# Kernel tuning notes

Hardware: AMD Instinct MI355X
Metric: run time of the kernel (lower is better)

Reference implementation:

```python
import jax, jax.numpy as jnp
import numpy as np

B, CI, HW, K, C, NH, L = 512, 3, 28, 28 // 28 and 0 or 7, 1024, 16, 12
K = 7


def setup_inputs() -> dict:
    key = jax.random.key(0)
    ks = jax.random.split(key, 8)
    s = 0.02
    return {
        "x": jax.random.normal(ks[0], (B, CI, HW, HW), jnp.float32),
        "conv_w": jax.random.normal(ks[1], (C, CI, K, K), jnp.float32) * s,  # Conv2d weight [Co,Ci,k,k], shared with deconv
        "ln1_w": jnp.ones((L, C), jnp.float32),
        "ln1_b": jnp.zeros((L, C), jnp.float32),
        "wq": jax.random.normal(ks[2], (L, C, C), jnp.float32) * s,
        "wk": jax.random.normal(ks[3], (L, C, C), jnp.float32) * s,
        "wv": jax.random.normal(ks[4], (L, C, C), jnp.float32) * s,
        "ln2_w": jnp.ones((L, C), jnp.float32),
        "ln2_b": jnp.zeros((L, C), jnp.float32),
        "mlp_w": jax.random.normal(ks[5], (L, C, C), jnp.float32) * s,
        "mlp_b": jnp.zeros((L, C), jnp.float32),
        "out_w": jax.random.normal(ks[6], (C, C), jnp.float32) * s,
        "out_b": jnp.zeros((C,), jnp.float32),
        "head_num": NH,
    }


def _layernorm(x, w, b, eps=1e-5):
    m = jnp.mean(x, axis=-1, keepdims=True)
    v = jnp.var(x, axis=-1, keepdims=True)  # biased var, matches torch LayerNorm
    return (x - m) * jax.lax.rsqrt(v + eps) * w + b


def _attn(h, wq, wk, wv, nh):
    b, t, c = h.shape
    hd = c // nh
    q = (h @ wq.T).reshape(b, t, nh, hd).transpose(0, 2, 1, 3)  # [B,H,T,hd]
    k = (h @ wk.T).reshape(b, t, nh, hd).transpose(0, 2, 1, 3)
    v = (h @ wv.T).reshape(b, t, nh, hd).transpose(0, 2, 1, 3)
    scores = jnp.einsum("bhqd,bhkd->bhqk", q, k) / jnp.sqrt(jnp.float32(hd))
    mask = jnp.tril(jnp.ones((t, t), bool))
    scores = jnp.where(mask, scores, -jnp.inf)
    a = jax.nn.softmax(scores, axis=-1)
    o = jnp.einsum("bhqk,bhkd->bhqd", a, v)
    return o.transpose(0, 2, 1, 3).reshape(b, t, c)


def _forward(x, conv_w, ln1_w, ln1_b, wq, wk, wv, ln2_w, ln2_b, mlp_w, mlp_b, out_w, out_b, head_num):
    b, ci, hh, ww = x.shape
    co, _, k, _ = conv_w.shape
    # thumbnail: bilinear downsample to (k,k) (align_corners=False == half-pixel), then k-strided conv -> [B,Co]
    thumb = jax.image.resize(x, (b, ci, k, k), method="bilinear", antialias=False)
    thumb_tok = jnp.einsum("bcpq,dcpq->bd", thumb, conv_w)
    # kernel==stride conv == patchify + matmul
    hp, wp = hh // k, ww // k
    xp = x.reshape(b, ci, hp, k, wp, k)
    patches = jnp.einsum("bcipjq,dcpq->bdij", xp, conv_w).reshape(b, co, hp * wp)
    h = jnp.concatenate([thumb_tok[:, :, None], patches], axis=-1).transpose(0, 2, 1)  # [B,T=1+hp*wp,C]
    nlayers = ln1_w.shape[0]
    for l in range(nlayers):
        a = _attn(_layernorm(h, ln1_w[l], ln1_b[l]), wq[l], wk[l], wv[l], head_num)
        h = h + a
        m = _layernorm(h, ln2_w[l], ln2_b[l]) @ mlp_w[l].T + mlp_b[l]
        h = h + m
    logits = h @ out_w.T + out_b  # [B,T,C]
    # decode: ConvTranspose2d(kernel=stride=k) with shared weight; input [B,Co,1,T] -> [B,Ci,k,T*k]
    z = logits.transpose(0, 2, 1)  # [B,Co,T]
    t = z.shape[-1]
    out = jnp.einsum("bcs,cdhw->bdhsw", z, conv_w).reshape(b, ci, k, t * k)
    return out


def reference(x, conv_w, ln1_w, ln1_b, wq, wk, wv, ln2_w, ln2_b, mlp_w, mlp_b, out_w, out_b, head_num):
    return _forward(x, conv_w, ln1_w, ln1_b, wq, wk, wv, ln2_w, ln2_b, mlp_w, mlp_b, out_w, out_b, head_num)
```

## Files before the change

kernel.cpp:

```cpp
#include <hip/hip_runtime.h>


typedef unsigned short u16;
typedef short bfrag8 __attribute__((ext_vector_type(8)));
typedef float facc4 __attribute__((ext_vector_type(4)));

__device__ __forceinline__ u16 f2bf(float f) {
  union { float f; unsigned u; } x; x.f = f;
  unsigned r = x.u + 0x7fffu + ((x.u >> 16) & 1u);
  return (u16)(r >> 16);
}
__device__ __forceinline__ float bf2f(u16 h) {
  union { unsigned u; float f; } x; x.u = ((unsigned)h) << 16;
  return x.f;
}

template <int MODE>
__global__ __launch_bounds__(256) void gemm_bt(
    const u16* __restrict__ A, int lda,
    const u16* __restrict__ B0, const u16* __restrict__ B1, const u16* __restrict__ B2,
    int ldb, int K,
    void* __restrict__ outp, long long zstride, int ldo,
    const float* __restrict__ bias)
{
  __shared__ __align__(16) u16 As[8192];
  __shared__ __align__(16) u16 Bs[8192];

  const int n0 = blockIdx.x * 128;
  const int m0 = blockIdx.y * 128;
  const int z  = blockIdx.z;
  const u16* __restrict__ B = (z == 0) ? B0 : ((z == 1) ? B1 : B2);

  const int tid  = threadIdx.x;
  const int wave = tid >> 6;
  const int lane = tid & 63;
  const int wm   = (wave >> 1) * 64;
  const int wn   = (wave & 1) * 64;
  const int lrow = lane & 15;
  const int lquad = lane >> 4;

  facc4 acc[4][4] = {};

  const u16* ga[4]; const u16* gb[4];
#pragma unroll
  for (int j = 0; j < 4; ++j) {
    const int s = tid + 256 * j;
    const int t = s >> 9, s2 = s & 511;
    const int r = s2 >> 2, c = (s2 & 3) + 4 * t;
    ga[j] = A + (long long)(m0 + r) * lda + c * 8;
    gb[j] = B + (long long)(n0 + r) * ldb + c * 8;
  }

  const int aoff = (wm + lrow) * 32 + lquad * 8;
  const int boff = (wn + lrow) * 32 + lquad * 8;

  for (int k0 = 0; k0 < K; k0 += 64) {
#pragma unroll
    for (int j = 0; j < 4; ++j) {
      __builtin_amdgcn_global_load_lds((const __attribute__((address_space(1))) void*)ga[j],
                                       (__attribute__((address_space(3))) void*)(As + (tid + 256 * j) * 8), 16, 0, 0);
      __builtin_amdgcn_global_load_lds((const __attribute__((address_space(1))) void*)gb[j],
                                       (__attribute__((address_space(3))) void*)(Bs + (tid + 256 * j) * 8), 16, 0, 0);
      ga[j] += 64; gb[j] += 64;
    }
    __syncthreads();

#pragma unroll
    for (int t = 0; t < 2; ++t) {
      bfrag8 af[4], bfr[4];
#pragma unroll
      for (int im = 0; im < 4; ++im) af[im] = *(const bfrag8*)(As + t * 4096 + aoff + 512 * im);
#pragma unroll
      for (int in = 0; in < 4; ++in) bfr[in] = *(const bfrag8*)(Bs + t * 4096 + boff + 512 * in);
#pragma unroll
      for (int im = 0; im < 4; ++im)
#pragma unroll
        for (int in = 0; in < 4; ++in)
          acc[im][in] = __builtin_amdgcn_mfma_f32_16x16x32_bf16(af[im], bfr[in], acc[im][in], 0, 0, 0);
    }
    __syncthreads();
  }

#pragma unroll
  for (int in = 0; in < 4; ++in) {
    const int col = n0 + wn + in * 16 + lrow;
    const float bb = (MODE != 3 && bias) ? bias[col] : 0.0f;
#pragma unroll
    for (int im = 0; im < 4; ++im) {
#pragma unroll
      for (int r = 0; r < 4; ++r) {
        const int row = m0 + wm + im * 16 + lquad * 4 + r;
        const float v = acc[im][in][r] + bb;
        if (MODE == 0) {
          ((float*)outp)[(long long)row * ldo + col] = v;
        } else if (MODE == 1) {
          (((u16*)outp) + zstride * z)[(long long)row * ldo + col] = f2bf(v);
        } else if (MODE == 2) {
          ((float*)outp)[(long long)row * ldo + col] += v;
        } else {
          if (col < 147) {
            const int b = row / 17, s = row - b * 17;
            const int d = col / 49, rem = col - d * 49;
            const int hk = rem / 7, wk = rem - hk * 7;
            ((float*)outp)[(long long)((b * 3 + d) * 7 + hk) * 119 + s * 7 + wk] = v;
          }
        }
      }
    }
  }
}

__global__ __launch_bounds__(256) void ln_kernel(
    const float* __restrict__ h, const float* __restrict__ w,
    const float* __restrict__ b, u16* __restrict__ out)
{
  const long long row = blockIdx.x;
  const float* __restrict__ x = h + row * 1024;
  const int t = threadIdx.x;
  float v0 = x[t], v1 = x[t + 256], v2 = x[t + 512], v3 = x[t + 768];
  float s = v0 + v1 + v2 + v3;
  float q = v0 * v0 + v1 * v1 + v2 * v2 + v3 * v3;
  for (int o = 32; o > 0; o >>= 1) { s += __shfl_down(s, o); q += __shfl_down(q, o); }
  __shared__ float ss[4], sq[4];
  const int wave = t >> 6, lane = t & 63;
  if (lane == 0) { ss[wave] = s; sq[wave] = q; }
  __syncthreads();
  const float st = ss[0] + ss[1] + ss[2] + ss[3];
  const float qt = sq[0] + sq[1] + sq[2] + sq[3];
  const float mean = st * (1.0f / 1024.0f);
  const float var = qt * (1.0f / 1024.0f) - mean * mean;
  const float inv = rsqrtf(var + 1e-5f);
  u16* o2 = out + row * 1024;
  o2[t]       = f2bf((v0 - mean) * inv * w[t]       + b[t]);
  o2[t + 256] = f2bf((v1 - mean) * inv * w[t + 256] + b[t + 256]);
  o2[t + 512] = f2bf((v2 - mean) * inv * w[t + 512] + b[t + 512]);
  o2[t + 768] = f2bf((v3 - mean) * inv * w[t + 768] + b[t + 768]);
}

__global__ __launch_bounds__(256) void attn_kernel(const u16* __restrict__ QKV,
                                                   float* __restrict__ h)
{
  const int blk = blockIdx.x;
  const int b = blk >> 4, head = blk & 15;
  __shared__ float qs[17][64], ks[17][64], vs[17][64];
  __shared__ float sc[17][20];
  const long long base = (long long)b * 17 * 1024 + head * 64;
  const u16* Q  = QKV;
  const u16* Kp = QKV + 8912896LL;
  const u16* V  = QKV + 17825792LL;

  for (int i = threadIdx.x; i < 17 * 64; i += 256) {
    const int t = i >> 6, d = i & 63;
    const long long off = base + (long long)t * 1024 + d;
    qs[t][d] = bf2f(Q[off]); ks[t][d] = bf2f(Kp[off]); vs[t][d] = bf2f(V[off]);
  }
  __syncthreads();

  for (int i = threadIdx.x; i < 289; i += 256) {
    const int tq = i / 17, tk = i % 17;
    float a = 0.0f;
    if (tk <= tq) {
#pragma unroll
      for (int d = 0; d < 64; ++d) a += qs[tq][d] * ks[tk][d];
      a *= 0.125f;
    }
    sc[tq][tk] = a;
  }
  __syncthreads();

  if (threadIdx.x < 17) {
    const int tq = threadIdx.x;
    float m = -1e30f;
    for (int tk = 0; tk <= tq; ++tk) m = fmaxf(m, sc[tq][tk]);
    float s = 0.0f;
    for (int tk = 0; tk <= tq; ++tk) { const float e = __expf(sc[tq][tk] - m); sc[tq][tk] = e; s += e; }
    const float inv = 1.0f / s;
    for (int tk = 0; tk <= tq; ++tk) sc[tq][tk] *= inv;
  }
  __syncthreads();

  for (int i = threadIdx.x; i < 17 * 64; i += 256) {
    const int tq = i >> 6, d = i & 63;
    float a = 0.0f;
    for (int tk = 0; tk <= tq; ++tk) a += sc[tq][tk] * vs[tk][d];
    h[base + (long long)tq * 1024 + d] += a;
  }
}

__global__ void build_p(const float* __restrict__ x, u16* __restrict__ P)
{
  const int n = blockIdx.x;
  const int j = threadIdx.x;
  if (j >= 192) return;
  const int b = n / 17, t = n % 17;
  float val = 0.0f;
  if (j < 147) {
    const int c = j / 49, rem = j % 49, p = rem / 7, q = rem % 7;
    const float* xb = x + (long long)(b * 3 + c) * 784;
    if (t == 0) {
      const int r = 4 * p + 1, cc = 4 * q + 1;
      val = 0.25f * (xb[r * 28 + cc] + xb[r * 28 + cc + 1] +
                     xb[(r + 1) * 28 + cc] + xb[(r + 1) * 28 + cc + 1]);
    } else {
      const int s = t - 1, ii = s >> 2, jj = s & 3;
      val = xb[(7 * ii + p) * 28 + 7 * jj + q];
    }
  }
  P[(long long)n * 192 + j] = f2bf(val);
}

__global__ __launch_bounds__(256) void cvt_conv(const float* __restrict__ cw,
                                                u16* __restrict__ Wc, u16* __restrict__ cw2)
{
  const int i = blockIdx.x * 256 + threadIdx.x;
  if (i < 196608) {
    const int d = i / 192, j = i % 192;
    Wc[i] = (j < 147) ? f2bf(cw[d * 147 + j]) : (u16)0;
  } else {
    const int i2 = i - 196608;
    if (i2 < 262144) {
      const int j = i2 / 1024, c = i2 % 1024;
      cw2[i2] = (j < 147) ? f2bf(cw[c * 147 + j]) : (u16)0;
    }
  }
}

__global__ __launch_bounds__(256) void cvt_all(
    const float* __restrict__ wq, const float* __restrict__ wk,
    const float* __restrict__ wv, const float* __restrict__ mlpw,
    const float* __restrict__ outw, u16* __restrict__ wAll)
{
  const int i = blockIdx.x * 256 + threadIdx.x;
  const int which = i >> 18;
  const int off = i & 262143;
  const float4* src;
  if (which < 48) {
    const int layer = which >> 2, sub = which & 3;
    const float* base = (sub == 0) ? wq : (sub == 1) ? wk : (sub == 2) ? wv : mlpw;
    src = (const float4*)(base + (size_t)layer * 1048576) + off;
  } else {
    src = (const float4*)outw + off;
  }
  const float4 v = *src;
  ushort4 o; o.x = f2bf(v.x); o.y = f2bf(v.y); o.z = f2bf(v.z); o.w = f2bf(v.w);
  *(ushort4*)(wAll + (size_t)which * 1048576 + (size_t)off * 4) = o;
}

__global__ __launch_bounds__(256) void cvt4(const float* __restrict__ a0, const float* __restrict__ a1,
                                            const float* __restrict__ a2, const float* __restrict__ a3,
                                            u16* __restrict__ o3, u16* __restrict__ om)
{
  const int i = blockIdx.x * 256 + threadIdx.x;
  const int which = i >> 20, off = i & 1048575;
  const float* src = (which == 0) ? a0 : (which == 1) ? a1 : (which == 2) ? a2 : a3;
  const float v = src[off];
  if (which < 3) o3[which * 1048576 + off] = f2bf(v);
  else           om[off] = f2bf(v);
}

__global__ __launch_bounds__(256) void cvtN(const float* __restrict__ in, u16* __restrict__ out, int n)
{
  const int i = blockIdx.x * 256 + threadIdx.x;
  if (i < n) out[i] = f2bf(in[i]);
}

extern "C" void kernel_launch(void* const* d_in, const int* in_sizes, int n_in,
                              void* d_out, int out_size, void* d_ws, size_t ws_size,
                              hipStream_t stream)
{
  const float* x     = (const float*)d_in[0];
  const float* convw = (const float*)d_in[1];
  const float* ln1w  = (const float*)d_in[2];
  const float* ln1b  = (const float*)d_in[3];
  const float* wq    = (const float*)d_in[4];
  const float* wk    = (const float*)d_in[5];
  const float* wv    = (const float*)d_in[6];
  const float* ln2w  = (const float*)d_in[7];
  const float* ln2b  = (const float*)d_in[8];
  const float* mlpw  = (const float*)d_in[9];
  const float* mlpb  = (const float*)d_in[10];
  const float* outw  = (const float*)d_in[11];
  const float* outb  = (const float*)d_in[12];

  char* w = (char*)d_ws;
  const bool big = (ws_size >= 213975040ULL);

  if (big) {
    float* h   = (float*)(w);
    u16* Abuf  = (u16*)(w + 35651584);
    u16* QKV   = (u16*)(w + 53477376);
    u16* wAll  = (u16*)(w + 106954752);
    u16* Wc    = (u16*)(w + 209715200);
    u16* cw2   = (u16*)(w + 210108416);
    u16* P     = (u16*)(w + 210632704);

    cvt_all<<<50176, 256, 0, stream>>>(wq, wk, wv, mlpw, outw, wAll);
    cvt_conv<<<1792, 256, 0, stream>>>(convw, Wc, cw2);
    build_p<<<8704, 192, 0, stream>>>(x, P);
    gemm_bt<0><<<dim3(8, 68, 1), 256, 0, stream>>>(P, 192, Wc, Wc, Wc, 192, 192,
                                                   (void*)h, 0LL, 1024, nullptr);
    for (int l = 0; l < 12; ++l) {
      u16* wl = wAll + (size_t)l * 4194304;
      ln_kernel<<<8704, 256, 0, stream>>>(h, ln1w + l * 1024, ln1b + l * 1024, Abuf);
      gemm_bt<1><<<dim3(8, 68, 3), 256, 0, stream>>>(Abuf, 1024, wl, wl + 1048576, wl + 2097152,
                                                     1024, 1024, (void*)QKV, 8912896LL, 1024, nullptr);
      attn_kernel<<<8192, 256, 0, stream>>>(QKV, h);
      ln_kernel<<<8704, 256, 0, stream>>>(h, ln2w + l * 1024, ln2b + l * 1024, Abuf);
      gemm_bt<2><<<dim3(8, 68, 1), 256, 0, stream>>>(Abuf, 1024, wl + 3145728, wl, wl,
                                                     1024, 1024, (void*)h, 0LL, 1024, mlpb + l * 1024);
    }
    u16* wout = wAll + (size_t)48 * 1048576;
    cvtN<<<34816, 256, 0, stream>>>(h, Abuf, 8912896);
    gemm_bt<1><<<dim3(8, 68, 1), 256, 0, stream>>>(Abuf, 1024, wout, wout, wout,
                                                   1024, 1024, (void*)QKV, 0LL, 1024, outb);
    gemm_bt<3><<<dim3(2, 68, 1), 256, 0, stream>>>(QKV, 1024, cw2, cw2, cw2,
                                                   1024, 1024, d_out, 0LL, 0, nullptr);
  } else {
    if (ws_size < 119603200ULL) return;
    float* h   = (float*)(w);
    u16* Abuf  = (u16*)(w + 35651584);
    u16* QKV   = (u16*)(w + 53477376);
    u16* wb3   = (u16*)(w + 106954752);
    u16* wmb   = (u16*)(w + 113246208);
    u16* Wc    = (u16*)(w + 115343360);
    u16* cw2   = (u16*)(w + 115736576);
    u16* P     = (u16*)(w + 116260864);

    cvt_conv<<<1792, 256, 0, stream>>>(convw, Wc, cw2);
    build_p<<<8704, 192, 0, stream>>>(x, P);
    gemm_bt<0><<<dim3(8, 68, 1), 256, 0, stream>>>(P, 192, Wc, Wc, Wc, 192, 192,
                                                   (void*)h, 0LL, 1024, nullptr);
    for (int l = 0; l < 12; ++l) {
      const size_t wo = (size_t)l * 1048576;
      cvt4<<<16384, 256, 0, stream>>>(wq + wo, wk + wo, wv + wo, mlpw + wo, wb3, wmb);
      ln_kernel<<<8704, 256, 0, stream>>>(h, ln1w + l * 1024, ln1b + l * 1024, Abuf);
      gemm_bt<1><<<dim3(8, 68, 3), 256, 0, stream>>>(Abuf, 1024, wb3, wb3 + 1048576, wb3 + 2097152,
                                                     1024, 1024, (void*)QKV, 8912896LL, 1024, nullptr);
      attn_kernel<<<8192, 256, 0, stream>>>(QKV, h);
      ln_kernel<<<8704, 256, 0, stream>>>(h, ln2w + l * 1024, ln2b + l * 1024, Abuf);
      gemm_bt<2><<<dim3(8, 68, 1), 256, 0, stream>>>(Abuf, 1024, wmb, wmb, wmb,
                                                     1024, 1024, (void*)h, 0LL, 1024, mlpb + l * 1024);
    }
    cvtN<<<34816, 256, 0, stream>>>(h, Abuf, 8912896);
    cvtN<<<4096, 256, 0, stream>>>(outw, wmb, 1048576);
    gemm_bt<1><<<dim3(8, 68, 1), 256, 0, stream>>>(Abuf, 1024, wmb, wmb, wmb,
                                                   1024, 1024, (void*)QKV, 0LL, 1024, outb);
    gemm_bt<3><<<dim3(2, 68, 1), 256, 0, stream>>>(QKV, 1024, cw2, cw2, cw2,
                                                   1024, 1024, d_out, 0LL, 0, nullptr);
  }
}
```

Baseline: 2.970 ms.

## Load MFMA fragments straight from global memory with register double buffering

Removes the LDS staging (global_load_lds plus two barriers per K step) from the bf16 GEMM. Each wave now loads its A/B fragments directly from global memory into registers and ping-pongs two register sets so the loads for the next K slice overlap the MFMAs on the current one. The aim is to drop the synchronisation and LDS traffic. In exchange there is no sharing of tiles between waves, so global/L2 traffic roughly doubles. Each lane also reads only 16 bytes per row, which is less coalesced. The loop assumes K/32 is even, which holds for K=1024 but may not for other sizes.

```diff
diff --git a/kernel.cpp b/kernel.cpp
--- a/kernel.cpp
+++ b/kernel.cpp
@@ -14,6 +14,23 @@
   union { unsigned u; float f; } x; x.u = ((unsigned)h) << 16;
   return x.f;
 }
+
+#define LOAD_SET(ab, bb)                                                    \
+  {                                                                         \
+    _Pragma("unroll")                                                       \
+    for (int im = 0; im < 4; ++im) { ab[im] = *(const bfrag8*)ap[im]; ap[im] += 32; } \
+    _Pragma("unroll")                                                       \
+    for (int in = 0; in < 4; ++in) { bb[in] = *(const bfrag8*)bp[in]; bp[in] += 32; } \
+  }
+
+#define MFMA_SET(ab, bb)                                                    \
+  {                                                                         \
+    _Pragma("unroll")                                                       \
+    for (int im = 0; im < 4; ++im)                                          \
+      _Pragma("unroll")                                                     \
+      for (int in = 0; in < 4; ++in)                                        \
+        acc[im][in] = __builtin_amdgcn_mfma_f32_16x16x32_bf16(ab[im], bb[in], acc[im][in], 0, 0, 0); \
+  }
 
 template <int MODE>
 __global__ __launch_bounds__(256) void gemm_bt(
@@ -23,9 +40,6 @@
     void* __restrict__ outp, long long zstride, int ldo,
     const float* __restrict__ bias)
 {
-  __shared__ __align__(16) u16 As[8192];
-  __shared__ __align__(16) u16 Bs[8192];
-
   const int n0 = blockIdx.x * 128;
   const int m0 = blockIdx.y * 128;
   const int z  = blockIdx.z;
@@ -41,45 +55,27 @@
 
   facc4 acc[4][4] = {};
 
-  const u16* ga[4]; const u16* gb[4];
-#pragma unroll
-  for (int j = 0; j < 4; ++j) {
-    const int s = tid + 256 * j;
-    const int t = s >> 9, s2 = s & 511;
-    const int r = s2 >> 2, c = (s2 & 3) + 4 * t;
-    ga[j] = A + (long long)(m0 + r) * lda + c * 8;
-    gb[j] = B + (long long)(n0 + r) * ldb + c * 8;
-  }
-
-  const int aoff = (wm + lrow) * 32 + lquad * 8;
-  const int boff = (wn + lrow) * 32 + lquad * 8;
-
-  for (int k0 = 0; k0 < K; k0 += 64) {
-#pragma unroll
-    for (int j = 0; j < 4; ++j) {
-      __builtin_amdgcn_global_load_lds((const __attribute__((address_space(1))) void*)ga[j],
-                                       (__attribute__((address_space(3))) void*)(As + (tid + 256 * j) * 8), 16, 0, 0);
-      __builtin_amdgcn_global_load_lds((const __attribute__((address_space(1))) void*)gb[j],
-                                       (__attribute__((address_space(3))) void*)(Bs + (tid + 256 * j) * 8), 16, 0, 0);
-      ga[j] += 64; gb[j] += 64;
-    }
-    __syncthreads();
-
-#pragma unroll
-    for (int t = 0; t < 2; ++t) {
-      bfrag8 af[4], bfr[4];
-#pragma unroll
-      for (int im = 0; im < 4; ++im) af[im] = *(const bfrag8*)(As + t * 4096 + aoff + 512 * im);
-#pragma unroll
-      for (int in = 0; in < 4; ++in) bfr[in] = *(const bfrag8*)(Bs + t * 4096 + boff + 512 * in);
-#pragma unroll
-      for (int im = 0; im < 4; ++im)
-#pragma unroll
-        for (int in = 0; in < 4; ++in)
-          acc[im][in] = __builtin_amdgcn_mfma_f32_16x16x32_bf16(af[im], bfr[in], acc[im][in], 0, 0, 0);
-    }
-    __syncthreads();
-  }
+  const u16* ap[4]; const u16* bp[4];
+#pragma unroll
+  for (int im = 0; im < 4; ++im)
+    ap[im] = A + (long long)(m0 + wm + im * 16 + lrow) * lda + lquad * 8;
+#pragma unroll
+  for (int in = 0; in < 4; ++in)
+    bp[in] = B + (long long)(n0 + wn + in * 16 + lrow) * ldb + lquad * 8;
+
+  bfrag8 a0[4], b0[4], a1[4], b1[4];
+  const int nIter = K >> 5;
+
+  LOAD_SET(a0, b0);
+  for (int i = 1; i + 1 < nIter; i += 2) {
+    LOAD_SET(a1, b1);
+    MFMA_SET(a0, b0);
+    LOAD_SET(a0, b0);
+    MFMA_SET(a1, b1);
+  }
+  LOAD_SET(a1, b1);
+  MFMA_SET(a0, b0);
+  MFMA_SET(a1, b1);
 
 #pragma unroll
   for (int in = 0; in < 4; ++in) {
```

Result: slower. 5.140 ms (+73.0%).

## Fold output projection into deconv weight and vectorize LN/attention memory access

Applied to the files above, without the earlier changes.

Precomputes W' = cw2·out_w and b' = cw2·out_b so the final 1024x1024 output GEMM is removed and the deconv GEMM consumes the last residual stream directly. The last MLP GEMM gets a new mode that writes both the fp32 residual and a bf16 copy, which also removes the separate conversion pass. LayerNorm and attention loads and stores are vectorized to float4/uint4. Folding the two projections changes where bf16 rounding happens and adds a small per-call weight-product kernel.

```diff
diff --git a/kernel.cpp b/kernel.cpp
--- a/kernel.cpp
+++ b/kernel.cpp
@@ -84,7 +84,7 @@
 #pragma unroll
   for (int in = 0; in < 4; ++in) {
     const int col = n0 + wn + in * 16 + lrow;
-    const float bb = (MODE != 3 && bias) ? bias[col] : 0.0f;
+    const float bb = bias ? bias[col] : 0.0f;
 #pragma unroll
     for (int im = 0; im < 4; ++im) {
 #pragma unroll
@@ -97,6 +97,11 @@
           (((u16*)outp) + zstride * z)[(long long)row * ldo + col] = f2bf(v);
         } else if (MODE == 2) {
           ((float*)outp)[(long long)row * ldo + col] += v;
+        } else if (MODE == 4) {
+          const long long off = (long long)row * ldo + col;
+          const float nv = ((float*)outp)[off] + v;
+          ((float*)outp)[off] = nv;
+          ((u16*)zstride)[off] = f2bf(nv);
         } else {
           if (col < 147) {
             const int b = row / 17, s = row - b * 17;
@@ -115,11 +120,10 @@
     const float* __restrict__ b, u16* __restrict__ out)
 {
   const long long row = blockIdx.x;
-  const float* __restrict__ x = h + row * 1024;
   const int t = threadIdx.x;
-  float v0 = x[t], v1 = x[t + 256], v2 = x[t + 512], v3 = x[t + 768];
-  float s = v0 + v1 + v2 + v3;
-  float q = v0 * v0 + v1 * v1 + v2 * v2 + v3 * v3;
+  const float4 v = ((const float4*)(h + row * 1024))[t];
+  float s = v.x + v.y + v.z + v.w;
+  float q = v.x * v.x + v.y * v.y + v.z * v.z + v.w * v.w;
   for (int o = 32; o > 0; o >>= 1) { s += __shfl_down(s, o); q += __shfl_down(q, o); }
   __shared__ float ss[4], sq[4];
   const int wave = t >> 6, lane = t & 63;
@@ -130,11 +134,14 @@
   const float mean = st * (1.0f / 1024.0f);
   const float var = qt * (1.0f / 1024.0f) - mean * mean;
   const float inv = rsqrtf(var + 1e-5f);
-  u16* o2 = out + row * 1024;
-  o2[t]       = f2bf((v0 - mean) * inv * w[t]       + b[t]);
-  o2[t + 256] = f2bf((v1 - mean) * inv * w[t + 256] + b[t + 256]);
-  o2[t + 512] = f2bf((v2 - mean) * inv * w[t + 512] + b[t + 512]);
-  o2[t + 768] = f2bf((v3 - mean) * inv * w[t + 768] + b[t + 768]);
+  const float4 w4 = ((const float4*)w)[t];
+  const float4 b4 = ((const float4*)b)[t];
+  ushort4 o;
+  o.x = f2bf((v.x - mean) * inv * w4.x + b4.x);
+  o.y = f2bf((v.y - mean) * inv * w4.y + b4.y);
+  o.z = f2bf((v.z - mean) * inv * w4.z + b4.z);
+  o.w = f2bf((v.w - mean) * inv * w4.w + b4.w);
+  ((ushort4*)(out + row * 1024))[t] = o;
 }
 
 __global__ __launch_bounds__(256) void attn_kernel(const u16* __restrict__ QKV,
@@ -144,19 +151,29 @@
   const int b = blk >> 4, head = blk & 15;
   __shared__ float qs[17][64], ks[17][64], vs[17][64];
   __shared__ float sc[17][20];
-  const long long base = (long long)b * 17 * 1024 + head * 64;
+  const long long base = (long long)b * 17408 + head * 64;
   const u16* Q  = QKV;
   const u16* Kp = QKV + 8912896LL;
   const u16* V  = QKV + 17825792LL;
-
-  for (int i = threadIdx.x; i < 17 * 64; i += 256) {
-    const int t = i >> 6, d = i & 63;
-    const long long off = base + (long long)t * 1024 + d;
-    qs[t][d] = bf2f(Q[off]); ks[t][d] = bf2f(Kp[off]); vs[t][d] = bf2f(V[off]);
+  const int tid = threadIdx.x;
+
+  if (tid < 136) {
+    const int t = tid >> 3, dg = (tid & 7) * 8;
+    const long long off = base + (long long)t * 1024 + dg;
+    union { uint4 u; u16 s[8]; } xq, xk, xv;
+    xq.u = *(const uint4*)(Q + off);
+    xk.u = *(const uint4*)(Kp + off);
+    xv.u = *(const uint4*)(V + off);
+#pragma unroll
+    for (int j = 0; j < 8; ++j) {
+      qs[t][dg + j] = bf2f(xq.s[j]);
+      ks[t][dg + j] = bf2f(xk.s[j]);
+      vs[t][dg + j] = bf2f(xv.s[j]);
+    }
   }
   __syncthreads();
 
-  for (int i = threadIdx.x; i < 289; i += 256) {
+  for (int i = tid; i < 289; i += 256) {
     const int tq = i / 17, tk = i % 17;
     float a = 0.0f;
     if (tk <= tq) {
@@ -168,8 +185,8 @@
   }
   __syncthreads();
 
-  if (threadIdx.x < 17) {
-    const int tq = threadIdx.x;
+  if (tid < 17) {
+    const int tq = tid;
     float m = -1e30f;
     for (int tk = 0; tk <= tq; ++tk) m = fmaxf(m, sc[tq][tk]);
     float s = 0.0f;
@@ -179,11 +196,18 @@
   }
   __syncthreads();
 
-  for (int i = threadIdx.x; i < 17 * 64; i += 256) {
-    const int tq = i >> 6, d = i & 63;
-    float a = 0.0f;
-    for (int tk = 0; tk <= tq; ++tk) a += sc[tq][tk] * vs[tk][d];
-    h[base + (long long)tq * 1024 + d] += a;
+  for (int i = tid; i < 272; i += 256) {
+    const int tq = i >> 4, dg = (i & 15) * 4;
+    float o0 = 0, o1 = 0, o2 = 0, o3 = 0;
+    for (int tk = 0; tk <= tq; ++tk) {
+      const float s = sc[tq][tk];
+      o0 += s * vs[tk][dg];     o1 += s * vs[tk][dg + 1];
+      o2 += s * vs[tk][dg + 2]; o3 += s * vs[tk][dg + 3];
+    }
+    float4* hp = (float4*)(h + base + (long long)tq * 1024 + dg);
+    float4 hv = *hp;
+    hv.x += o0; hv.y += o1; hv.z += o2; hv.w += o3;
+    *hp = hv;
   }
 }
 
@@ -225,6 +249,28 @@
   }
 }
 
+__global__ __launch_bounds__(256) void wprime_kernel(
+    const u16* __restrict__ cw2, const float* __restrict__ outw,
+    u16* __restrict__ Wp)
+{
+  const int k = blockIdx.x * 256 + threadIdx.x;
+  const int j = blockIdx.y;
+  float a = 0.0f;
+  for (int c = 0; c < 1024; ++c)
+    a += bf2f(cw2[j * 1024 + c]) * outw[c * 1024 + k];
+  Wp[j * 1024 + k] = f2bf(a);
+}
+
+__global__ __launch_bounds__(256) void bprime_kernel(
+    const u16* __restrict__ cw2, const float* __restrict__ outb,
+    float* __restrict__ bp)
+{
+  const int j = threadIdx.x;
+  float a = 0.0f;
+  for (int c = 0; c < 1024; ++c) a += outb[c] * bf2f(cw2[j * 1024 + c]);
+  bp[j] = a;
+}
+
 __global__ __launch_bounds__(256) void cvt_all(
     const float* __restrict__ wq, const float* __restrict__ wk,
     const float* __restrict__ wv, const float* __restrict__ mlpw,
@@ -283,7 +329,7 @@
   const float* outb  = (const float*)d_in[12];
 
   char* w = (char*)d_ws;
-  const bool big = (ws_size >= 213975040ULL);
+  const bool big = (ws_size >= 214500352ULL);
 
   if (big) {
     float* h   = (float*)(w);
@@ -293,9 +339,13 @@
     u16* Wc    = (u16*)(w + 209715200);
     u16* cw2   = (u16*)(w + 210108416);
     u16* P     = (u16*)(w + 210632704);
+    u16* Wp    = (u16*)(w + 213975040);
+    float* bp  = (float*)(w + 214499328);
 
     cvt_all<<<50176, 256, 0, stream>>>(wq, wk, wv, mlpw, outw, wAll);
     cvt_conv<<<1792, 256, 0, stream>>>(convw, Wc, cw2);
+    wprime_kernel<<<dim3(4, 256), 256, 0, stream>>>(cw2, outw, Wp);
+    bprime_kernel<<<1, 256, 0, stream>>>(cw2, outb, bp);
     build_p<<<8704, 192, 0, stream>>>(x, P);
     gemm_bt<0><<<dim3(8, 68, 1), 256, 0, stream>>>(P, 192, Wc, Wc, Wc, 192, 192,
                                                    (void*)h, 0LL, 1024, nullptr);
@@ -306,15 +356,18 @@
                                                      1024, 1024, (void*)QKV, 8912896LL, 1024, nullptr);
       attn_kernel<<<8192, 256, 0, stream>>>(QKV, h);
       ln_kernel<<<8704, 256, 0, stream>>>(h, ln2w + l * 1024, ln2b + l * 1024, Abuf);
-      gemm_bt<2><<<dim3(8, 68, 1), 256, 0, stream>>>(Abuf, 1024, wl + 3145728, wl, wl,
-                                                     1024, 1024, (void*)h, 0LL, 1024, mlpb + l * 1024);
-    }
-    u16* wout = wAll + (size_t)48 * 1048576;
-    cvtN<<<34816, 256, 0, stream>>>(h, Abuf, 8912896);
-    gemm_bt<1><<<dim3(8, 68, 1), 256, 0, stream>>>(Abuf, 1024, wout, wout, wout,
-                                                   1024, 1024, (void*)QKV, 0LL, 1024, outb);
-    gemm_bt<3><<<dim3(2, 68, 1), 256, 0, stream>>>(QKV, 1024, cw2, cw2, cw2,
-                                                   1024, 1024, d_out, 0LL, 0, nullptr);
+      if (l < 11) {
+        gemm_bt<2><<<dim3(8, 68, 1), 256, 0, stream>>>(Abuf, 1024, wl + 3145728, wl, wl,
+                                                       1024, 1024, (void*)h, 0LL, 1024, mlpb + l * 1024);
+      } else {
+        gemm_bt<4><<<dim3(8, 68, 1), 256, 0, stream>>>(Abuf, 1024, wl + 3145728, wl, wl,
+                                                       1024, 1024, (void*)h,
+                                                       (long long)(uintptr_t)QKV, 1024,
+                                                       mlpb + l * 1024);
+      }
+    }
+    gemm_bt<3><<<dim3(2, 68, 1), 256, 0, stream>>>(QKV, 1024, Wp, Wp, Wp,
+                                                   1024, 1024, d_out, 0LL, 0, bp);
   } else {
     if (ws_size < 119603200ULL) return;
     float* h   = (float*)(w);
```

Measured after the change: 2.957 ms. About the same (-0.4%).
